# Kernel optimization log

Hardware: AMD Instinct MI355X
Metric: run time of the kernel (lower is better)

The kernel has to match this reference:

```python
import jax, jax.numpy as jnp
import numpy as np

N = 50000      # num nodes
E = 800000     # num edges (before self-loops)
DIN = 256
DOUT = 256
K = 3


def setup_inputs() -> dict:
    key = jax.random.key(0)
    k1, k2, k3 = jax.random.split(key, 3)
    x = jax.random.normal(k1, (N, DIN), dtype=jnp.float32)
    edge_index = jax.random.randint(k2, (2, E), 0, N, dtype=jnp.int32)
    # xavier_uniform for weight [K+1, DIN, DOUT]
    limit = float(np.sqrt(6.0 / (DIN + DOUT)))
    weight = jax.random.uniform(k3, (K + 1, DIN, DOUT), dtype=jnp.float32,
                                minval=-limit, maxval=limit)
    bias = jnp.zeros((DOUT,), dtype=jnp.float32)
    return {"x": x, "edge_index": edge_index, "weight": weight, "bias": bias}


def reference(x, edge_index, weight, bias):
    num_nodes = x.shape[0]
    # add self loops
    loops = jnp.arange(num_nodes, dtype=edge_index.dtype)
    row = jnp.concatenate([edge_index[0], loops])
    col = jnp.concatenate([edge_index[1], loops])
    # degree of row (including self loops)
    deg = jax.ops.segment_sum(jnp.ones_like(row, dtype=x.dtype), row,
                              num_segments=num_nodes)
    deg_inv_sqrt = jnp.where(deg > 0, jax.lax.rsqrt(jnp.maximum(deg, 1e-30)), 0.0)
    # edge-weighted Laplacian values: -D^{-1/2} A D^{-1/2}, +1 on diagonal
    Lvals = -deg_inv_sqrt[row] * deg_inv_sqrt[col]
    Lvals = jnp.where(row == col, Lvals + 1.0, Lvals)

    def spmm(v):  # [N, D] -> [N, D]
        return jax.ops.segment_sum(Lvals[:, None] * v[col], row,
                                   num_segments=num_nodes)

    out = jnp.matmul(x, weight[0])
    Tx_0 = x
    Tx_1 = spmm(x)
    out = out + jnp.matmul(Tx_1, weight[1])
    for k in range(2, K + 1):
        Tx_2 = 2.0 * spmm(Tx_1) - Tx_0
        out = out + jnp.matmul(Tx_2, weight[k])
        Tx_0, Tx_1 = Tx_1, Tx_2
    return out + bias
```

## Files before the change

kernel.cpp:

```cpp
#include <hip/hip_runtime.h>
#include <hip/hip_bf16.h>

#define DFEAT 256
#define RSTRIDE 64

typedef __attribute__((ext_vector_type(8))) short bf16x8;
typedef __attribute__((ext_vector_type(4))) float f32x4;

__device__ __forceinline__ float bf2f(unsigned short u) {
  return __builtin_bit_cast(float, ((unsigned)u) << 16);
}
__device__ __forceinline__ unsigned short f2bf(float f) {
  __hip_bfloat16 h = __float2bfloat16(f);
  return *reinterpret_cast<unsigned short*>(&h);
}
__device__ __forceinline__ void gload_lds16(const void* g, void* l) {
  __builtin_amdgcn_global_load_lds(
      (const __attribute__((address_space(1))) void*)g,
      (__attribute__((address_space(3))) void*)l, 16, 0, 0);
}


__global__ void k_build(const int* __restrict__ ei0, const int* __restrict__ ei1, int E,
                        int* __restrict__ cnt, int* __restrict__ colsP) {
  int i = blockIdx.x * blockDim.x + threadIdx.x;
  if (i >= E) return;
  int r = ei0[i];
  int pos = atomicAdd(&cnt[r], 1);
  if (pos < RSTRIDE) colsP[(size_t)r * RSTRIDE + pos] = ei1[i];
}


__global__ __launch_bounds__(256) void k_f2bfwt(const float* __restrict__ x,
                                                unsigned short* __restrict__ xbf, int n4,
                                                const float* __restrict__ W,
                                                unsigned short* __restrict__ WT,
                                                const int* __restrict__ cnt,
                                                float* __restrict__ dis, int N, int nb) {
  int b = blockIdx.x;
  if (b < 256) {
    int idx = b * 256 + threadIdx.x;
    int n = idx & 255;
    int k = idx >> 8;
    float w0 = W[idx];
    float w1 = W[65536 + idx];
    float w2 = W[2 * 65536 + idx];
    float w3 = W[3 * 65536 + idx];
    int t = (n << 8) | k;
    WT[t]             = f2bf(w0 - w2);
    WT[65536 + t]     = f2bf(w1 - 3.0f * w3);
    WT[2 * 65536 + t] = f2bf(2.0f * w2);
    WT[3 * 65536 + t] = f2bf(4.0f * w3);
    return;
  }
  if (b < 256 + nb) {
    int i = (b - 256) * 256 + threadIdx.x;
    if (i < N) dis[i] = rsqrtf((float)(cnt[i] + 1));
    return;
  }
  int i = (b - 256 - nb) * 256 + threadIdx.x;
  if (i >= n4) return;
  float4 f = *(const float4*)(x + (size_t)i * 4);
  ushort4 u;
  u.x = f2bf(f.x); u.y = f2bf(f.y); u.z = f2bf(f.z); u.w = f2bf(f.w);
  *(ushort4*)(xbf + (size_t)i * 4) = u;
}


__global__ __launch_bounds__(256) void k_spmm_bf(
    const unsigned short* __restrict__ v, unsigned short* __restrict__ y,
    const int* __restrict__ cnt, const int* __restrict__ colsP,
    const float* __restrict__ dis, int N) {
  int r = blockIdx.x * 4 + (threadIdx.x >> 6);
  if (r >= N) return;
  int lane = threadIdx.x & 63;
  int fo = lane * 4;
  int len = cnt[r];
  if (len > RSTRIDE) len = RSTRIDE;
  const int* cp = colsP + (size_t)r * RSTRIDE;
  float dr = dis[r];
  float a0 = 0.f, a1 = 0.f, a2 = 0.f, a3 = 0.f;

  int e = 0;
  for (; e + 3 < len; e += 4) {
    int c0 = cp[e], c1 = cp[e + 1], c2 = cp[e + 2], c3 = cp[e + 3];
    float l0 = -dr * dis[c0] + (c0 == r ? 1.f : 0.f);
    float l1 = -dr * dis[c1] + (c1 == r ? 1.f : 0.f);
    float l2 = -dr * dis[c2] + (c2 == r ? 1.f : 0.f);
    float l3 = -dr * dis[c3] + (c3 == r ? 1.f : 0.f);
    uint2 u0 = *(const uint2*)(v + (size_t)c0 * DFEAT + fo);
    uint2 u1 = *(const uint2*)(v + (size_t)c1 * DFEAT + fo);
    uint2 u2 = *(const uint2*)(v + (size_t)c2 * DFEAT + fo);
    uint2 u3 = *(const uint2*)(v + (size_t)c3 * DFEAT + fo);
    a0 += l0 * bf2f(u0.x & 0xffff) + l1 * bf2f(u1.x & 0xffff) +
          l2 * bf2f(u2.x & 0xffff) + l3 * bf2f(u3.x & 0xffff);
    a1 += l0 * bf2f(u0.x >> 16) + l1 * bf2f(u1.x >> 16) +
          l2 * bf2f(u2.x >> 16) + l3 * bf2f(u3.x >> 16);
    a2 += l0 * bf2f(u0.y & 0xffff) + l1 * bf2f(u1.y & 0xffff) +
          l2 * bf2f(u2.y & 0xffff) + l3 * bf2f(u3.y & 0xffff);
    a3 += l0 * bf2f(u0.y >> 16) + l1 * bf2f(u1.y >> 16) +
          l2 * bf2f(u2.y >> 16) + l3 * bf2f(u3.y >> 16);
  }
  for (; e < len; ++e) {
    int c = cp[e];
    float lv = -dr * dis[c] + (c == r ? 1.f : 0.f);
    uint2 u = *(const uint2*)(v + (size_t)c * DFEAT + fo);
    a0 += lv * bf2f(u.x & 0xffff);
    a1 += lv * bf2f(u.x >> 16);
    a2 += lv * bf2f(u.y & 0xffff);
    a3 += lv * bf2f(u.y >> 16);
  }

  float sc = 1.0f - dr * dr;
  uint2 uv = *(const uint2*)(v + (size_t)r * DFEAT + fo);
  a0 += sc * bf2f(uv.x & 0xffff);
  a1 += sc * bf2f(uv.x >> 16);
  a2 += sc * bf2f(uv.y & 0xffff);
  a3 += sc * bf2f(uv.y >> 16);

  uint2 o;
  o.x = (unsigned)f2bf(a0) | ((unsigned)f2bf(a1) << 16);
  o.y = (unsigned)f2bf(a2) | ((unsigned)f2bf(a3) << 16);
  *(uint2*)(y + (size_t)r * DFEAT + fo) = o;
}


__global__ __launch_bounds__(256) void k_gemm4(
    const unsigned short* __restrict__ A0, const unsigned short* __restrict__ A1,
    const unsigned short* __restrict__ A2, const unsigned short* __restrict__ A3,
    const unsigned short* __restrict__ WT,
    const float* __restrict__ bias, float* __restrict__ C, int N) {
  __shared__ __align__(16) unsigned short lds[2][320 * 32];
  int tid = threadIdx.x;
  int lane = tid & 63;
  int w = tid >> 6;
  int brow = blockIdx.x * 64;

  f32x4 acc[4][4] = {};

  int lrow = lane >> 2;
  int selem = ((lane & 3) ^ ((lrow >> 1) & 3)) << 3;

  auto stage = [&](int buf, int it) {
    int g = it >> 3;
    int k0 = (it & 7) * 32;
    const unsigned short* Asrc = g == 0 ? A0 : g == 1 ? A1 : g == 2 ? A2 : A3;
    const unsigned short* Bsrc = WT + (g << 16);
#pragma unroll
    for (int c = 0; c < 5; ++c) {
      int gr = c * 64 + w * 16 + lrow;
      const unsigned short* src;
      if (gr < 64) {
        int grow = brow + gr;
        if (grow >= N) grow = N - 1;
        src = Asrc + (size_t)grow * DFEAT + k0 + selem;
      } else {
        src = Bsrc + (size_t)(gr - 64) * DFEAT + k0 + selem;
      }
      gload_lds16(src, (char*)lds[buf] + (c * 64 + w * 16) * 64);
    }
  };

  stage(0, 0);
  __syncthreads();

  for (int it = 0; it < 32; ++it) {
    int cur = it & 1;
    if (it < 31) stage(cur ^ 1, it + 1);
    bf16x8 af[4], bfr[4];
#pragma unroll
    for (int i = 0; i < 4; ++i) {
      int row = i * 16 + (lane & 15);
      int kb = ((lane >> 4) << 4) ^ (((row >> 1) & 3) << 4);
      af[i] = *(const bf16x8*)((const char*)lds[cur] + row * 64 + kb);
    }
#pragma unroll
    for (int j = 0; j < 4; ++j) {
      int n = w * 64 + j * 16 + (lane & 15);
      int row = 64 + n;
      int kb = ((lane >> 4) << 4) ^ (((row >> 1) & 3) << 4);
      bfr[j] = *(const bf16x8*)((const char*)lds[cur] + row * 64 + kb);
    }
    __builtin_amdgcn_s_setprio(1);
#pragma unroll
    for (int i = 0; i < 4; ++i)
#pragma unroll
      for (int j = 0; j < 4; ++j)
        acc[i][j] = __builtin_amdgcn_mfma_f32_16x16x32_bf16(af[i], bfr[j], acc[i][j], 0, 0, 0);
    __builtin_amdgcn_s_setprio(0);
    if (it < 31) __syncthreads();
  }

#pragma unroll
  for (int i = 0; i < 4; ++i) {
    int rowb = brow + i * 16 + (lane >> 4) * 4;
#pragma unroll
    for (int j = 0; j < 4; ++j) {
      int col = w * 64 + j * 16 + (lane & 15);
      float b = bias[col];
#pragma unroll
      for (int q = 0; q < 4; ++q) {
        int r = rowb + q;
        if (r < N) C[(size_t)r * DFEAT + col] = acc[i][j][q] + b;
      }
    }
  }
}


extern "C" void kernel_launch(void* const* d_in, const int* in_sizes, int n_in,
                              void* d_out, int out_size, void* d_ws, size_t ws_size,
                              hipStream_t stream) {
  const float* x = (const float*)d_in[0];
  const int* ei = (const int*)d_in[1];
  const float* weight = (const float*)d_in[2];
  const float* bias = (const float*)d_in[3];
  float* out = (float*)d_out;

  int N = in_sizes[0] / DFEAT;
  int E = in_sizes[1] / 2;
  const int* ei0 = ei;
  const int* ei1 = ei + E;

  char* ws = (char*)d_ws;
  size_t off = 0;
  auto alloc = [&](size_t bytes) {
    void* p = ws + off;
    off = (off + bytes + 255) & ~(size_t)255;
    return p;
  };
  int* cnt = (int*)alloc((size_t)N * sizeof(int));
  float* dis = (float*)alloc((size_t)N * sizeof(float));
  int* colsP = (int*)alloc((size_t)N * RSTRIDE * sizeof(int));
  unsigned short* xbf = (unsigned short*)alloc((size_t)N * DFEAT * 2);
  unsigned short* S1 = (unsigned short*)alloc((size_t)N * DFEAT * 2);
  unsigned short* S2 = (unsigned short*)alloc((size_t)N * DFEAT * 2);
  unsigned short* S3 = (unsigned short*)alloc((size_t)N * DFEAT * 2);
  unsigned short* WT = (unsigned short*)alloc((size_t)4 * DFEAT * DFEAT * 2);

  hipMemsetAsync(cnt, 0, (size_t)N * sizeof(int), stream);

  int eb = (E + 255) / 256;
  int nb = (N + 255) / 256;
  int n4 = N * DFEAT / 4;
  k_build<<<eb, 256, 0, stream>>>(ei0, ei1, E, cnt, colsP);
  k_f2bfwt<<<256 + nb + (n4 + 255) / 256, 256, 0, stream>>>(x, xbf, n4, weight, WT,
                                                            cnt, dis, N, nb);

  int sgrid = (N + 3) / 4;
  k_spmm_bf<<<sgrid, 256, 0, stream>>>(xbf, S1, cnt, colsP, dis, N);
  k_spmm_bf<<<sgrid, 256, 0, stream>>>(S1, S2, cnt, colsP, dis, N);
  k_spmm_bf<<<sgrid, 256, 0, stream>>>(S2, S3, cnt, colsP, dis, N);

  int ggrid = (N + 63) / 64;
  k_gemm4<<<ggrid, 256, 0, stream>>>(xbf, S1, S2, S3, WT, bias, out, N);
}
```

Before: 304.5 us.

## Load GEMM operands directly from global memory instead of LDS staging

The fused 4-way GEMM drops its double-buffered LDS staging (global_load_lds plus barriers). Each lane now reads its bf16x8 A and B fragments straight from global memory into registers, with all 32 k-steps fully unrolled. This removes the LDS traffic, the swizzling and the __syncthreads, and relies on L1/L2 caching for reuse across waves. The cost is redundant global reads (B is reloaded per block, A is reloaded by all four waves), with no explicit prefetch to hide latency.

```diff
diff --git a/kernel.cpp b/kernel.cpp
--- a/kernel.cpp
+++ b/kernel.cpp
@@ -13,11 +13,6 @@
 __device__ __forceinline__ unsigned short f2bf(float f) {
   __hip_bfloat16 h = __float2bfloat16(f);
   return *reinterpret_cast<unsigned short*>(&h);
-}
-__device__ __forceinline__ void gload_lds16(const void* g, void* l) {
-  __builtin_amdgcn_global_load_lds(
-      (const __attribute__((address_space(1))) void*)g,
-      (__attribute__((address_space(3))) void*)l, 16, 0, 0);
 }
 
 
@@ -130,65 +125,49 @@
     const unsigned short* __restrict__ A2, const unsigned short* __restrict__ A3,
     const unsigned short* __restrict__ WT,
     const float* __restrict__ bias, float* __restrict__ C, int N) {
-  __shared__ __align__(16) unsigned short lds[2][320 * 32];
   int tid = threadIdx.x;
   int lane = tid & 63;
   int w = tid >> 6;
   int brow = blockIdx.x * 64;
+  int arow = lane & 15;
+  int kslot = (lane >> 4) * 8;
 
   f32x4 acc[4][4] = {};
 
-  int lrow = lane >> 2;
-  int selem = ((lane & 3) ^ ((lrow >> 1) & 3)) << 3;
-
-  auto stage = [&](int buf, int it) {
-    int g = it >> 3;
-    int k0 = (it & 7) * 32;
+  const unsigned short* bptr[4];
+#pragma unroll
+  for (int j = 0; j < 4; ++j)
+    bptr[j] = WT + (size_t)(w * 64 + j * 16 + arow) * DFEAT + kslot;
+
+#pragma unroll
+  for (int g = 0; g < 4; ++g) {
     const unsigned short* Asrc = g == 0 ? A0 : g == 1 ? A1 : g == 2 ? A2 : A3;
-    const unsigned short* Bsrc = WT + (g << 16);
-#pragma unroll
-    for (int c = 0; c < 5; ++c) {
-      int gr = c * 64 + w * 16 + lrow;
-      const unsigned short* src;
-      if (gr < 64) {
-        int grow = brow + gr;
-        if (grow >= N) grow = N - 1;
-        src = Asrc + (size_t)grow * DFEAT + k0 + selem;
-      } else {
-        src = Bsrc + (size_t)(gr - 64) * DFEAT + k0 + selem;
-      }
-      gload_lds16(src, (char*)lds[buf] + (c * 64 + w * 16) * 64);
+    const unsigned short* aptr[4];
+#pragma unroll
+    for (int i = 0; i < 4; ++i) {
+      int r = brow + i * 16 + arow;
+      if (r >= N) r = N - 1;
+      aptr[i] = Asrc + (size_t)r * DFEAT + kslot;
     }
-  };
-
-  stage(0, 0);
-  __syncthreads();
-
-  for (int it = 0; it < 32; ++it) {
-    int cur = it & 1;
-    if (it < 31) stage(cur ^ 1, it + 1);
-    bf16x8 af[4], bfr[4];
-#pragma unroll
-    for (int i = 0; i < 4; ++i) {
-      int row = i * 16 + (lane & 15);
-      int kb = ((lane >> 4) << 4) ^ (((row >> 1) & 3) << 4);
-      af[i] = *(const bf16x8*)((const char*)lds[cur] + row * 64 + kb);
+    const unsigned short* bg = (const unsigned short*)((const char*)0);
+#pragma unroll
+    for (int ks = 0; ks < 8; ++ks) {
+      bf16x8 af[4], bfr[4];
+#pragma unroll
+      for (int i = 0; i < 4; ++i)
+        af[i] = *(const bf16x8*)(aptr[i] + ks * 32);
+#pragma unroll
+      for (int j = 0; j < 4; ++j)
+        bfr[j] = *(const bf16x8*)(bptr[j] + (size_t)g * 65536 + ks * 32);
+      __builtin_amdgcn_s_setprio(1);
+#pragma unroll
+      for (int i = 0; i < 4; ++i)
+#pragma unroll
+        for (int j = 0; j < 4; ++j)
+          acc[i][j] = __builtin_amdgcn_mfma_f32_16x16x32_bf16(af[i], bfr[j], acc[i][j], 0, 0, 0);
+      __builtin_amdgcn_s_setprio(0);
     }
-#pragma unroll
-    for (int j = 0; j < 4; ++j) {
-      int n = w * 64 + j * 16 + (lane & 15);
-      int row = 64 + n;
-      int kb = ((lane >> 4) << 4) ^ (((row >> 1) & 3) << 4);
-      bfr[j] = *(const bf16x8*)((const char*)lds[cur] + row * 64 + kb);
-    }
-    __builtin_amdgcn_s_setprio(1);
-#pragma unroll
-    for (int i = 0; i < 4; ++i)
-#pragma unroll
-      for (int j = 0; j < 4; ++j)
-        acc[i][j] = __builtin_amdgcn_mfma_f32_16x16x32_bf16(af[i], bfr[j], acc[i][j], 0, 0, 0);
-    __builtin_amdgcn_s_setprio(0);
-    if (it < 31) __syncthreads();
+    (void)bg;
   }
 
 #pragma unroll
```

Measured after the change: 367.1 us. 1.21x slower.
